# Performance work log

Hardware: AMD Instinct MI355X
Metric: run time of the kernel (lower is better)

## Reference

```python
import jax, jax.numpy as jnp
import numpy as np


def gcn_conv(x, edge_index, edge_weight, W, b):
    """Faithful PyG GCNConv: add self-loops (weight 1), symmetric normalization,
    linear transform, weighted sum aggregation at target nodes, then bias."""
    N = x.shape[0]
    loops = jnp.arange(N, dtype=edge_index.dtype)
    row = jnp.concatenate([edge_index[0], loops])  # source j
    col = jnp.concatenate([edge_index[1], loops])  # target i
    ew = jnp.concatenate([edge_weight, jnp.ones((N,), dtype=edge_weight.dtype)])
    deg = jax.ops.segment_sum(ew, col, num_segments=N)  # [N]
    dinv = jnp.where(deg > 0, jax.lax.rsqrt(deg), 0.0)
    norm = dinv[row] * ew * dinv[col]  # [E+N]
    xw = x @ W  # [N, F_out]
    msgs = xw[row] * norm[:, None]  # [E+N, F_out]
    out = jax.ops.segment_sum(msgs, col, num_segments=N)  # [N, F_out]
    return out + b


def setup_inputs() -> dict:
    key = jax.random.key(0)
    k = jax.random.split(key, 8)
    N, E, Fin, Fhid, Fout = 50000, 800000, 128, 128, 64
    x = jax.random.normal(k[0], (N, Fin), dtype=jnp.float32)
    edge_index = jax.random.randint(k[1], (2, E), 0, N, dtype=jnp.int64)
    edge_weight = jax.random.uniform(k[2], (E,), dtype=jnp.float32)
    s0 = 1.0 / np.sqrt(Fin)
    s1 = 1.0 / np.sqrt(Fhid)
    W0 = jax.random.uniform(k[3], (Fin, Fhid), jnp.float32, -s0, s0)
    b0 = jnp.zeros((Fhid,), jnp.float32)
    W1 = jax.random.uniform(k[4], (Fhid, Fout), jnp.float32, -s1, s1)
    b1 = jnp.zeros((Fout,), jnp.float32)
    return {"x": x, "edge_index": edge_index, "edge_weight": edge_weight,
            "W0": W0, "b0": b0, "W1": W1, "b1": b1}


def reference(x, edge_index, edge_weight, W0, b0, W1, b1):
    # Encoder with num_layers=2, drop_p=0.0 (identity), activation=ReLU
    h = gcn_conv(x, edge_index, edge_weight, W0, b0)
    h = jax.nn.relu(h)
    h = gcn_conv(h, edge_index, edge_weight, W1, b1)
    h = jax.nn.relu(h)
    return h
```

## Files before the change

### kernel.cpp

```cpp
#include <hip/hip_runtime.h>

#define MAXDEG 48
#define BSH 6
#define BNODES 64
#define BCAP 2048

typedef unsigned short ushort_t;
typedef __attribute__((ext_vector_type(8))) short short8;
typedef __attribute__((ext_vector_type(4))) float f32x4;

__device__ inline ushort_t f2bf(float f) {
    union { float f; unsigned u; } v;
    v.f = f;
    unsigned r = v.u + 0x7fff + ((v.u >> 16) & 1);
    return (ushort_t)(r >> 16);
}

__device__ inline float bf2f_lo(unsigned u) {
    union { unsigned u; float f; } v;
    v.u = u << 16;
    return v.f;
}

__device__ inline float bf2f_hi(unsigned u) {
    union { unsigned u; float f; } v;
    v.u = u & 0xffff0000u;
    return v.f;
}


__global__ void k_setup(const float* __restrict__ W0, ushort_t* __restrict__ wp0,
                        const float* __restrict__ W1, ushort_t* __restrict__ wp1,
                        int* __restrict__ bcur, int NB) {
    int tid = blockIdx.x * blockDim.x + threadIdx.x;
    int stride = gridDim.x * blockDim.x;
    for (int i = tid; i < NB; i += stride) bcur[i] = 0;
    for (int e = tid; e < 16384; e += stride) {
        int j = e & 7, l = (e >> 3) & 63, ct = e >> 9;
        int t = ct & 7, c = ct >> 3;
        int k = 32 * c + (l >> 4) * 8 + j;
        int n = 16 * t + (l & 15);
        wp0[e] = f2bf(W0[k * 128 + n]);
    }
    for (int e = tid; e < 8192; e += stride) {
        int j = e & 7, l = (e >> 3) & 63, ct = e >> 9;
        int t = ct & 3, c = ct >> 2;
        int k = 32 * c + (l >> 4) * 8 + j;
        int n = 16 * t + (l & 15);
        wp1[e] = f2bf(W1[k * 64 + n]);
    }
}


__global__ __launch_bounds__(256) void k_scatter(const int* __restrict__ row,
                                                 const int* __restrict__ col,
                                                 const float* __restrict__ ew,
                                                 int* __restrict__ bcur,
                                                 uint2* __restrict__ recs, int E, int NB) {
    __shared__ int cnt[1024];
    __shared__ int base[1024];
    const int t = threadIdx.x;
    const size_t e0 = (size_t)blockIdx.x * (256 * 16);
    for (int i = t; i < NB; i += 256) cnt[i] = 0;
    __syncthreads();
    int ck[16], rk[16];
#pragma unroll
    for (int j = 0; j < 16; ++j) {
        size_t e = e0 + (size_t)j * 256 + t;
        ck[j] = -1;
        if (e < (size_t)E) {
            int c = col[e];
            ck[j] = c;
            rk[j] = atomicAdd(&cnt[c >> BSH], 1);
        }
    }
    __syncthreads();
    for (int i = t; i < NB; i += 256) {
        int c = cnt[i];
        base[i] = c ? atomicAdd(&bcur[i], c) : 0;
    }
    __syncthreads();
#pragma unroll
    for (int j = 0; j < 16; ++j) {
        size_t e = e0 + (size_t)j * 256 + t;
        if (e < (size_t)E) {
            int c = ck[j];
            int b = c >> BSH;
            int idx = base[b] + rk[j];
            if (idx < BCAP) {
                uint2 r;
                r.x = (unsigned)row[e] | ((unsigned)(c & (BNODES - 1)) << 16);
                r.y = __float_as_uint(ew[e]);
                recs[(size_t)b * BCAP + idx] = r;
            }
        }
    }
}


__global__ __launch_bounds__(256) void k_ell_build(const uint2* __restrict__ recs,
                                                   const int* __restrict__ bcur,
                                                   uint2* __restrict__ ell,
                                                   int* __restrict__ counts,
                                                   float* __restrict__ dinv, int N) {
    __shared__ uint2 tile[BNODES * MAXDEG];
    __shared__ int cnt[BNODES];
    const int b = blockIdx.x;
    const int t = threadIdx.x;
    if (t < BNODES) cnt[t] = 0;
    __syncthreads();
    const size_t s = (size_t)b * BCAP;
    const int ne = min(bcur[b], BCAP);
    for (int i = t; i < ne; i += 256) {
        uint2 r = recs[s + i];
        int dl = (r.x >> 16) & (BNODES - 1);
        int pos = atomicAdd(&cnt[dl], 1);
        if (pos < MAXDEG) {
            uint2 c;
            c.x = r.x & 0xffffu;
            c.y = r.y;
            tile[dl * MAXDEG + pos] = c;
        }
    }
    __syncthreads();
    const int node0 = b << BSH;
    if (t < BNODES) {
        int node = node0 + t;
        if (node < N) {
            int cn = min(cnt[t], MAXDEG);
            float sum = 1.0f;
            for (int j = 0; j < cn; ++j) sum += __uint_as_float(tile[t * MAXDEG + j].y);
            dinv[node] = rsqrtf(sum);
            counts[node] = cn;
        }
    }
    __syncthreads();
    const int nvalid = min(BNODES, N - node0);
    const int total = nvalid * MAXDEG;
    for (int i = t; i < total; i += 256) {
        int nl = i / MAXDEG;
        int slot = i - nl * MAXDEG;
        if (slot < min(cnt[nl], MAXDEG))
            ell[(size_t)node0 * MAXDEG + i] = tile[i];
    }
}


template <int FO, bool ABF16>
__global__ __launch_bounds__(256) void k_gemm_mfma(const void* __restrict__ Xv,
                                                   const uint4* __restrict__ Wp,
                                                   ushort_t* __restrict__ Y, int N) {
    constexpr int NT = FO >> 4;
    const int wave = threadIdx.x >> 6;
    const int lane = threadIdx.x & 63;
    const int m0 = blockIdx.x * 64 + wave * 16;
    if (m0 >= N) return;
    const int q = lane >> 4;
    const int mr = lane & 15;
    const int rowc = min(m0 + mr, N - 1);

    short8 a[4];
    if (ABF16) {
        const ushort_t* xr = (const ushort_t*)Xv + (size_t)rowc * 128 + q * 8;
#pragma unroll
        for (int c = 0; c < 4; ++c) {
            uint4 v = *(const uint4*)(xr + 32 * c);
            __builtin_memcpy(&a[c], &v, 16);
        }
    } else {
        const float* xr = (const float*)Xv + (size_t)rowc * 128 + q * 8;
#pragma unroll
        for (int c = 0; c < 4; ++c) {
            float4 v0 = *(const float4*)(xr + 32 * c);
            float4 v1 = *(const float4*)(xr + 32 * c + 4);
            a[c][0] = (short)f2bf(v0.x); a[c][1] = (short)f2bf(v0.y);
            a[c][2] = (short)f2bf(v0.z); a[c][3] = (short)f2bf(v0.w);
            a[c][4] = (short)f2bf(v1.x); a[c][5] = (short)f2bf(v1.y);
            a[c][6] = (short)f2bf(v1.z); a[c][7] = (short)f2bf(v1.w);
        }
    }

#pragma unroll
    for (int t = 0; t < NT; ++t) {
        f32x4 acc = {0.0f, 0.0f, 0.0f, 0.0f};
#pragma unroll
        for (int c = 0; c < 4; ++c) {
            uint4 bw = Wp[(size_t)(c * NT + t) * 64 + lane];
            short8 b;
            __builtin_memcpy(&b, &bw, 16);
            acc = __builtin_amdgcn_mfma_f32_16x16x32_bf16(a[c], b, acc, 0, 0, 0);
        }
        const int colbase = 16 * t + mr;
#pragma unroll
        for (int r = 0; r < 4; ++r) {
            int orow = m0 + q * 4 + r;
            if (orow < N) Y[(size_t)orow * FO + colbase] = f2bf(acc[r]);
        }
    }
}


__global__ __launch_bounds__(256) void k_gather128(const int* __restrict__ counts,
                                                   const uint2* __restrict__ ell,
                                                   const float* __restrict__ dinv,
                                                   const unsigned* __restrict__ xwb,
                                                   const float* __restrict__ bias,
                                                   unsigned* __restrict__ h1b, int N) {
    int node = (blockIdx.x * 256 + threadIdx.x) >> 6;
    int lane = threadIdx.x & 63;
    if (node >= N) return;
    float di = dinv[node];
    int cnt = min(counts[node], MAXDEG);

    int sv = 0;
    float wv = 0.0f;
    if (lane < cnt) {
        uint2 rec = ell[(size_t)node * MAXDEG + lane];
        sv = (int)rec.x;
        wv = dinv[sv] * __uint_as_float(rec.y) * di;
    }

    unsigned u0 = xwb[(size_t)node * 64 + lane];
    float2 bb = ((const float2*)bias)[lane];
    float sw = di * di;
    float ax = bb.x + bf2f_lo(u0) * sw;
    float ay = bb.y + bf2f_hi(u0) * sw;

    int j = 0;
    for (; j + 4 <= cnt; j += 4) {
        int s0 = __shfl(sv, j), s1 = __shfl(sv, j + 1), s2 = __shfl(sv, j + 2), s3 = __shfl(sv, j + 3);
        float w0 = __shfl(wv, j), w1 = __shfl(wv, j + 1), w2 = __shfl(wv, j + 2), w3 = __shfl(wv, j + 3);
        unsigned v0 = xwb[(size_t)s0 * 64 + lane];
        unsigned v1 = xwb[(size_t)s1 * 64 + lane];
        unsigned v2 = xwb[(size_t)s2 * 64 + lane];
        unsigned v3 = xwb[(size_t)s3 * 64 + lane];
        ax += bf2f_lo(v0) * w0; ay += bf2f_hi(v0) * w0;
        ax += bf2f_lo(v1) * w1; ay += bf2f_hi(v1) * w1;
        ax += bf2f_lo(v2) * w2; ay += bf2f_hi(v2) * w2;
        ax += bf2f_lo(v3) * w3; ay += bf2f_hi(v3) * w3;
    }
    for (; j < cnt; ++j) {
        int s = __shfl(sv, j);
        float w = __shfl(wv, j);
        unsigned v = xwb[(size_t)s * 64 + lane];
        ax += bf2f_lo(v) * w; ay += bf2f_hi(v) * w;
    }
    unsigned packed = ((unsigned)f2bf(fmaxf(ay, 0.0f)) << 16) | f2bf(fmaxf(ax, 0.0f));
    h1b[(size_t)node * 64 + lane] = packed;
}


__global__ __launch_bounds__(256) void k_gather64_relu(const int* __restrict__ counts,
                                                       const uint2* __restrict__ ell,
                                                       const float* __restrict__ dinv,
                                                       const ushort_t* __restrict__ xwb,
                                                       const float* __restrict__ bias,
                                                       float* __restrict__ h, int N) {
    int node = (blockIdx.x * 256 + threadIdx.x) >> 6;
    int lane = threadIdx.x & 63;
    if (node >= N) return;
    float di = dinv[node];
    int cnt = min(counts[node], MAXDEG);

    int sv = 0;
    float wv = 0.0f;
    if (lane < cnt) {
        uint2 rec = ell[(size_t)node * MAXDEG + lane];
        sv = (int)rec.x;
        wv = dinv[sv] * __uint_as_float(rec.y) * di;
    }

    float acc = bias[lane] + bf2f_lo((unsigned)xwb[(size_t)node * 64 + lane]) * di * di;

    int j = 0;
    for (; j + 4 <= cnt; j += 4) {
        int s0 = __shfl(sv, j), s1 = __shfl(sv, j + 1), s2 = __shfl(sv, j + 2), s3 = __shfl(sv, j + 3);
        float w0 = __shfl(wv, j), w1 = __shfl(wv, j + 1), w2 = __shfl(wv, j + 2), w3 = __shfl(wv, j + 3);
        float v0 = bf2f_lo((unsigned)xwb[(size_t)s0 * 64 + lane]);
        float v1 = bf2f_lo((unsigned)xwb[(size_t)s1 * 64 + lane]);
        float v2 = bf2f_lo((unsigned)xwb[(size_t)s2 * 64 + lane]);
        float v3 = bf2f_lo((unsigned)xwb[(size_t)s3 * 64 + lane]);
        acc += v0 * w0 + v1 * w1 + v2 * w2 + v3 * w3;
    }
    for (; j < cnt; ++j) {
        acc += bf2f_lo((unsigned)xwb[(size_t)__shfl(sv, j) * 64 + lane]) * __shfl(wv, j);
    }
    h[(size_t)node * 64 + lane] = fmaxf(acc, 0.0f);
}


extern "C" void kernel_launch(void* const* d_in, const int* in_sizes, int n_in,
                              void* d_out, int out_size, void* d_ws, size_t ws_size,
                              hipStream_t stream) {
    const float* x  = (const float*)d_in[0];
    const int*   ei = (const int*)d_in[1];
    const float* ew = (const float*)d_in[2];
    const float* W0 = (const float*)d_in[3];
    const float* b0 = (const float*)d_in[4];
    const float* W1 = (const float*)d_in[5];
    const float* b1 = (const float*)d_in[6];
    float* out = (float*)d_out;

    const int Fhid = in_sizes[4];
    const int Fin  = in_sizes[3] / Fhid;
    const int N    = in_sizes[0] / Fin;
    const int E    = in_sizes[2];
    const int NB   = (N + BNODES - 1) >> BSH;

    const int* row = ei;
    const int* col = ei + E;

    char* w = (char*)d_ws;
    auto alloc = [&](size_t bytes) {
        char* p = w;
        w += (bytes + 255) & ~(size_t)255;
        return p;
    };
    float*    dinv   = (float*)alloc((size_t)N * 4);
    int*      counts = (int*)alloc((size_t)N * 4);
    int*      bcur   = (int*)alloc((size_t)NB * 4);
    uint2*    recs   = (uint2*)alloc((size_t)NB * BCAP * 8);
    uint2*    ell    = (uint2*)alloc((size_t)N * MAXDEG * 8);
    ushort_t* xw1b   = (ushort_t*)alloc((size_t)N * 128 * 2);
    unsigned* h1b    = (unsigned*)alloc((size_t)N * 64 * 4);
    ushort_t* xw2b   = (ushort_t*)alloc((size_t)N * 64 * 2);
    ushort_t* wp0    = (ushort_t*)alloc(16384 * 2);
    ushort_t* wp1    = (ushort_t*)alloc(8192 * 2);

    const int T = 256;

    k_setup<<<32, T, 0, stream>>>(W0, wp0, W1, wp1, bcur, NB);
    k_scatter<<<(E + 4095) / 4096, T, 0, stream>>>(row, col, ew, bcur, recs, E, NB);
    k_ell_build<<<NB, T, 0, stream>>>(recs, bcur, ell, counts, dinv, N);

    const int GB = (N + 63) / 64;

    k_gemm_mfma<128, false><<<GB, T, 0, stream>>>(x, (const uint4*)wp0, xw1b, N);
    k_gather128<<<(N + 3) / 4, T, 0, stream>>>(counts, ell, dinv, (const unsigned*)xw1b, b0, h1b, N);

    k_gemm_mfma<64, true><<<GB, T, 0, stream>>>(h1b, (const uint4*)wp1, xw2b, N);
    k_gather64_relu<<<(N + 3) / 4, T, 0, stream>>>(counts, ell, dinv, xw2b, b1, out, N);
}
```

Before: 190.3 us.

## Split layer-2 gather into half-warps over edges; unroll layer-1 gather by eight

The layer-2 gather now has each half of the 64-lane wavefront handle a different edge. Each lane loads a packed pair of bf16 features (32 lanes cover 64 features), and the two halves are combined with a cross-half shuffle. This doubles the bytes per load and halves the serial loop length. The layer-1 gather gets an 8-way unrolled loop so more independent loads are in flight. Scatter records are stored as single 64-bit words, and source indices are masked to 16 bits, which is an extra safety op.

```diff
diff --git a/kernel.cpp b/kernel.cpp
--- a/kernel.cpp
+++ b/kernel.cpp
@@ -6,6 +6,7 @@
 #define BCAP 2048
 
 typedef unsigned short ushort_t;
+typedef unsigned long long u64_t;
 typedef __attribute__((ext_vector_type(8))) short short8;
 typedef __attribute__((ext_vector_type(4))) float f32x4;
 
@@ -56,7 +57,7 @@
                                                  const int* __restrict__ col,
                                                  const float* __restrict__ ew,
                                                  int* __restrict__ bcur,
-                                                 uint2* __restrict__ recs, int E, int NB) {
+                                                 u64_t* __restrict__ recs, int E, int NB) {
     __shared__ int cnt[1024];
     __shared__ int base[1024];
     const int t = threadIdx.x;
@@ -88,9 +89,8 @@
             int b = c >> BSH;
             int idx = base[b] + rk[j];
             if (idx < BCAP) {
-                uint2 r;
-                r.x = (unsigned)row[e] | ((unsigned)(c & (BNODES - 1)) << 16);
-                r.y = __float_as_uint(ew[e]);
+                u64_t r = (u64_t)((unsigned)row[e] | ((unsigned)(c & (BNODES - 1)) << 16))
+                          | ((u64_t)__float_as_uint(ew[e]) << 32);
                 recs[(size_t)b * BCAP + idx] = r;
             }
         }
@@ -98,7 +98,7 @@
 }
 
 
-__global__ __launch_bounds__(256) void k_ell_build(const uint2* __restrict__ recs,
+__global__ __launch_bounds__(256) void k_ell_build(const u64_t* __restrict__ recs,
                                                    const int* __restrict__ bcur,
                                                    uint2* __restrict__ ell,
                                                    int* __restrict__ counts,
@@ -112,13 +112,14 @@
     const size_t s = (size_t)b * BCAP;
     const int ne = min(bcur[b], BCAP);
     for (int i = t; i < ne; i += 256) {
-        uint2 r = recs[s + i];
-        int dl = (r.x >> 16) & (BNODES - 1);
+        u64_t r = recs[s + i];
+        unsigned rx = (unsigned)r;
+        int dl = (rx >> 16) & (BNODES - 1);
         int pos = atomicAdd(&cnt[dl], 1);
         if (pos < MAXDEG) {
             uint2 c;
-            c.x = r.x & 0xffffu;
-            c.y = r.y;
+            c.x = rx & 0xffffu;
+            c.y = (unsigned)(r >> 32);
             tile[dl * MAXDEG + pos] = c;
         }
     }
@@ -216,7 +217,7 @@
     float wv = 0.0f;
     if (lane < cnt) {
         uint2 rec = ell[(size_t)node * MAXDEG + lane];
-        sv = (int)rec.x;
+        sv = (int)(rec.x & 0xffffu);
         wv = dinv[sv] * __uint_as_float(rec.y) * di;
     }
 
@@ -227,6 +228,28 @@
     float ay = bb.y + bf2f_hi(u0) * sw;
 
     int j = 0;
+    for (; j + 8 <= cnt; j += 8) {
+        int s0 = __shfl(sv, j), s1 = __shfl(sv, j + 1), s2 = __shfl(sv, j + 2), s3 = __shfl(sv, j + 3);
+        int s4 = __shfl(sv, j + 4), s5 = __shfl(sv, j + 5), s6 = __shfl(sv, j + 6), s7 = __shfl(sv, j + 7);
+        float w0 = __shfl(wv, j), w1 = __shfl(wv, j + 1), w2 = __shfl(wv, j + 2), w3 = __shfl(wv, j + 3);
+        float w4 = __shfl(wv, j + 4), w5 = __shfl(wv, j + 5), w6 = __shfl(wv, j + 6), w7 = __shfl(wv, j + 7);
+        unsigned v0 = xwb[(size_t)s0 * 64 + lane];
+        unsigned v1 = xwb[(size_t)s1 * 64 + lane];
+        unsigned v2 = xwb[(size_t)s2 * 64 + lane];
+        unsigned v3 = xwb[(size_t)s3 * 64 + lane];
+        unsigned v4 = xwb[(size_t)s4 * 64 + lane];
+        unsigned v5 = xwb[(size_t)s5 * 64 + lane];
+        unsigned v6 = xwb[(size_t)s6 * 64 + lane];
+        unsigned v7 = xwb[(size_t)s7 * 64 + lane];
+        ax += bf2f_lo(v0) * w0; ay += bf2f_hi(v0) * w0;
+        ax += bf2f_lo(v1) * w1; ay += bf2f_hi(v1) * w1;
+        ax += bf2f_lo(v2) * w2; ay += bf2f_hi(v2) * w2;
+        ax += bf2f_lo(v3) * w3; ay += bf2f_hi(v3) * w3;
+        ax += bf2f_lo(v4) * w4; ay += bf2f_hi(v4) * w4;
+        ax += bf2f_lo(v5) * w5; ay += bf2f_hi(v5) * w5;
+        ax += bf2f_lo(v6) * w6; ay += bf2f_hi(v6) * w6;
+        ax += bf2f_lo(v7) * w7; ay += bf2f_hi(v7) * w7;
+    }
     for (; j + 4 <= cnt; j += 4) {
         int s0 = __shfl(sv, j), s1 = __shfl(sv, j + 1), s2 = __shfl(sv, j + 2), s3 = __shfl(sv, j + 3);
         float w0 = __shfl(wv, j), w1 = __shfl(wv, j + 1), w2 = __shfl(wv, j + 2), w3 = __shfl(wv, j + 3);
@@ -253,12 +276,14 @@
 __global__ __launch_bounds__(256) void k_gather64_relu(const int* __restrict__ counts,
                                                        const uint2* __restrict__ ell,
                                                        const float* __restrict__ dinv,
-                                                       const ushort_t* __restrict__ xwb,
+                                                       const unsigned* __restrict__ xwb,
                                                        const float* __restrict__ bias,
-                                                       float* __restrict__ h, int N) {
+                                                       float* __restrict__ out, int N) {
     int node = (blockIdx.x * 256 + threadIdx.x) >> 6;
     int lane = threadIdx.x & 63;
     if (node >= N) return;
+    const int half = lane >> 5;
+    const int fl = lane & 31;
     float di = dinv[node];
     int cnt = min(counts[node], MAXDEG);
 
@@ -266,26 +291,40 @@
     float wv = 0.0f;
     if (lane < cnt) {
         uint2 rec = ell[(size_t)node * MAXDEG + lane];
-        sv = (int)rec.x;
+        sv = (int)(rec.x & 0xffffu);
         wv = dinv[sv] * __uint_as_float(rec.y) * di;
     }
 
-    float acc = bias[lane] + bf2f_lo((unsigned)xwb[(size_t)node * 64 + lane]) * di * di;
-
+    float ax = 0.0f, ay = 0.0f;
     int j = 0;
-    for (; j + 4 <= cnt; j += 4) {
-        int s0 = __shfl(sv, j), s1 = __shfl(sv, j + 1), s2 = __shfl(sv, j + 2), s3 = __shfl(sv, j + 3);
-        float w0 = __shfl(wv, j), w1 = __shfl(wv, j + 1), w2 = __shfl(wv, j + 2), w3 = __shfl(wv, j + 3);
-        float v0 = bf2f_lo((unsigned)xwb[(size_t)s0 * 64 + lane]);
-        float v1 = bf2f_lo((unsigned)xwb[(size_t)s1 * 64 + lane]);
-        float v2 = bf2f_lo((unsigned)xwb[(size_t)s2 * 64 + lane]);
-        float v3 = bf2f_lo((unsigned)xwb[(size_t)s3 * 64 + lane]);
-        acc += v0 * w0 + v1 * w1 + v2 * w2 + v3 * w3;
-    }
-    for (; j < cnt; ++j) {
-        acc += bf2f_lo((unsigned)xwb[(size_t)__shfl(sv, j) * 64 + lane]) * __shfl(wv, j);
-    }
-    h[(size_t)node * 64 + lane] = fmaxf(acc, 0.0f);
+    for (; j + 2 <= cnt; j += 2) {
+        int e = j + half;
+        int s = __shfl(sv, e);
+        float w = __shfl(wv, e);
+        unsigned v = xwb[(size_t)s * 32 + fl];
+        ax += bf2f_lo(v) * w;
+        ay += bf2f_hi(v) * w;
+    }
+    if (j < cnt) {
+        int e = j + half;
+        int s = __shfl(sv, e);
+        float w = __shfl(wv, e);
+        unsigned v = xwb[(size_t)s * 32 + fl];
+        ax += bf2f_lo(v) * w;
+        ay += bf2f_hi(v) * w;
+    }
+    ax += __shfl_xor(ax, 32);
+    ay += __shfl_xor(ay, 32);
+
+    if (half == 0) {
+        unsigned u0 = xwb[(size_t)node * 32 + fl];
+        float2 bb = ((const float2*)bias)[fl];
+        float sw = di * di;
+        float2 r;
+        r.x = fmaxf(bb.x + bf2f_lo(u0) * sw + ax, 0.0f);
+        r.y = fmaxf(bb.y + bf2f_hi(u0) * sw + ay, 0.0f);
+        ((float2*)out)[(size_t)node * 32 + fl] = r;
+    }
 }
 
 
@@ -319,7 +358,7 @@
     float*    dinv   = (float*)alloc((size_t)N * 4);
     int*      counts = (int*)alloc((size_t)N * 4);
     int*      bcur   = (int*)alloc((size_t)NB * 4);
-    uint2*    recs   = (uint2*)alloc((size_t)NB * BCAP * 8);
+    u64_t*    recs   = (u64_t*)alloc((size_t)NB * BCAP * 8);
     uint2*    ell    = (uint2*)alloc((size_t)N * MAXDEG * 8);
     ushort_t* xw1b   = (ushort_t*)alloc((size_t)N * 128 * 2);
     unsigned* h1b    = (unsigned*)alloc((size_t)N * 64 * 4);
@@ -339,5 +378,5 @@
     k_gather128<<<(N + 3) / 4, T, 0, stream>>>(counts, ell, dinv, (const unsigned*)xw1b, b0, h1b, N);
 
     k_gemm_mfma<64, true><<<GB, T, 0, stream>>>(h1b, (const uint4*)wp1, xw2b, N);
-    k_gather64_relu<<<(N + 3) / 4, T, 0, stream>>>(counts, ell, dinv, xw2b, b1, out, N);
-}
+    k_gather64_relu<<<(N + 3) / 4, T, 0, stream>>>(counts, ell, dinv, (const unsigned*)xw2b, b1, out, N);
+}
```

Result: no change. 194.0 us (+2.0%).
